# Optimization experiments

Hardware: AMD Instinct MI355X
Metric: run time of the kernel (lower is better)

The kernel has to match this reference:

```python
import jax, jax.numpy as jnp
import numpy as np
import math

N, L, D = 1024, 32, 768
N_OUT, IN_DIM, OUT_DIM = 16, 64, 64
EPS = 1e-8


def setup_inputs() -> dict:
    key = jax.random.key(0)
    ks = jax.random.split(key, 4)
    x = jax.random.normal(ks[0], (N, L, D), jnp.float32)
    mask = jnp.ones((N, L), jnp.float32)
    scaled = lambda k, shape, fan: jax.random.normal(k, shape, jnp.float32) * (1.0 / np.sqrt(fan).astype(np.float32))
    Wscore = scaled(ks[1], (L, D, 1), D)
    Bscore = jnp.zeros((L, 1, 1), jnp.float32)
    Wcap = scaled(ks[2], (L, D, IN_DIM), D)
    Bcap = jnp.zeros((L, 1, IN_DIM), jnp.float32)
    Wvote = scaled(ks[3], (L, N_OUT, IN_DIM, OUT_DIM), IN_DIM)
    Bvote = jnp.zeros((L, N_OUT, 1, OUT_DIM), jnp.float32)
    beta_use = jnp.zeros((L, 1, 1, 1), jnp.float32)
    beta_ign = jnp.zeros((1, N_OUT, 1, 1), jnp.float32)
    return dict(x=x, mask=mask, Wscore=Wscore, Bscore=Bscore, Wcap=Wcap,
                Bcap=Bcap, Wvote=Wvote, Bvote=Bvote, beta_use=beta_use,
                beta_ign=beta_ign, iters=3)


def reference(x, mask, Wscore, Bscore, Wcap, Bcap, Wvote, Bvote, beta_use, beta_ign, iters):
    n_out = Wvote.shape[1]
    half_pi = np.float32(0.5 * math.pi)
    x_t = jnp.transpose(x, (1, 0, 2))                      # [L, N, D]
    a_in = jnp.matmul(x_t, Wscore) + Bscore                # [L, N, 1]
    mu_in = jax.nn.gelu(jnp.matmul(x_t, Wcap) + Bcap, approximate=False)  # [L, N, in_dim]
    f_a_in = jax.nn.sigmoid(a_in) * jnp.transpose(mask)[..., None]        # [L, N, 1]
    f_a_in = f_a_in[:, None, :, :]                         # [L, 1, N, 1]
    # votes: [L, n_out, N, out_dim] (einsum avoids materializing repeated mu_in)
    V = jnp.einsum('lni,lkio->lkno', mu_in, Wvote) + Bvote

    R = jnp.full((1, n_out, 1, 1), 1.0 / n_out, dtype=x.dtype)
    a_out = mu_out = var_out = None
    for t in range(iters):
        if t > 0:
            log_p = (-jnp.sum((V - mu_out[None]) ** 2 / (2.0 * var_out[None] + EPS), axis=-1)
                     - 1.0 - half_pi
                     - 0.5 * jnp.sum(jnp.log(var_out[None] + EPS), axis=-1))   # [L, n_out, N]
            R = jax.nn.softmax(jax.nn.log_sigmoid(a_out)[None] + log_p[..., None], axis=1)
        D_use = f_a_in * R                                  # [L, n_out, N, 1]
        D_ign = f_a_in - D_use
        a_out = jnp.sum(beta_use * D_use, axis=0) - jnp.sum(beta_ign * D_ign, axis=0)  # [n_out, N, 1]
        denom = jnp.sum(D_use, axis=0) + EPS                # [n_out, N, 1]
        mu_out = jnp.sum(D_use * V, axis=0) / denom         # [n_out, N, out_dim]
        var_out = jnp.sum(D_use * (V - mu_out[None]) ** 2, axis=0) / denom

    a_fin = jnp.transpose(a_out[..., 0])                    # [N, n_out]
    mu_fin = jnp.transpose(mu_out, (1, 0, 2))               # [N, n_out, out_dim]
    return a_fin, mu_fin
```

## Files before the change

kernel.cpp:

```cpp
#include <hip/hip_runtime.h>
#include <hip/hip_bf16.h>

#define L_DIM 32
#define N_DIM 1024
#define D_DIM 768
#define K_DIM 16
#define I_DIM 64
#define O_DIM 64
#define EPSF 1e-8f
#define PX 72

typedef unsigned short u16;
typedef __attribute__((ext_vector_type(8))) short short8;
typedef __attribute__((ext_vector_type(4))) float f32x4;
#define MFMA __builtin_amdgcn_mfma_f32_16x16x32_bf16

__device__ __forceinline__ float bf2f(u16 v) {
    union { unsigned int u; float f; } x; x.u = ((unsigned int)v) << 16; return x.f;
}
__device__ __forceinline__ u16 f2bf(float f) {
    union { float f; unsigned int u; } x; x.f = f;
    unsigned int u = x.u;
    u += 0x7FFFu + ((u >> 16) & 1u);
    return (u16)(u >> 16);
}
__device__ __forceinline__ void split2(float v, u16& h, u16& l) {
    u16 hh = f2bf(v);
    h = hh;
    l = f2bf(v - bf2f(hh));
}
__device__ __forceinline__ void store_split4(u16* ph, u16* pl, float4 v) {
    unsigned u0 = __float_as_uint(v.x), u1 = __float_as_uint(v.y);
    unsigned u2 = __float_as_uint(v.z), u3 = __float_as_uint(v.w);
    uint2 H, L;
    H.x = (u0 >> 16) | (u1 & 0xFFFF0000u);
    H.y = (u2 >> 16) | (u3 & 0xFFFF0000u);
    float l0 = v.x - __uint_as_float(u0 & 0xFFFF0000u);
    float l1 = v.y - __uint_as_float(u1 & 0xFFFF0000u);
    float l2 = v.z - __uint_as_float(u2 & 0xFFFF0000u);
    float l3 = v.w - __uint_as_float(u3 & 0xFFFF0000u);
    L.x = (__float_as_uint(l0) >> 16) | (__float_as_uint(l1) & 0xFFFF0000u);
    L.y = (__float_as_uint(l2) >> 16) | (__float_as_uint(l3) & 0xFFFF0000u);
    *(uint2*)ph = H;
    *(uint2*)pl = L;
}

__global__ __launch_bounds__(256) void prep_wcap(
    const float* __restrict__ W, u16* __restrict__ H, u16* __restrict__ Lo)
{
    const int l = blockIdx.y, d0 = blockIdx.x * 64, t = threadIdx.x;
    __shared__ float tile[64][65];
    #pragma unroll
    for (int p = 0; p < 4; p++) {
        int dd = p * 16 + (t >> 4), i4 = (t & 15) * 4;
        float4 v = *(const float4*)&W[((size_t)l * D_DIM + d0 + dd) * I_DIM + i4];
        tile[dd][i4] = v.x; tile[dd][i4+1] = v.y; tile[dd][i4+2] = v.z; tile[dd][i4+3] = v.w;
    }
    __syncthreads();
    #pragma unroll
    for (int p = 0; p < 4; p++) {
        int i = p * 16 + (t >> 4), dd0 = (t & 15) * 4;
        u16 h[4], lo[4];
        #pragma unroll
        for (int j = 0; j < 4; j++) split2(tile[dd0 + j][i], h[j], lo[j]);
        size_t base = ((size_t)l * I_DIM + i) * D_DIM + d0 + dd0;
        uint2 ph; ph.x = h[0] | ((unsigned)h[1] << 16); ph.y = h[2] | ((unsigned)h[3] << 16);
        uint2 pl; pl.x = lo[0] | ((unsigned)lo[1] << 16); pl.y = lo[2] | ((unsigned)lo[3] << 16);
        *(uint2*)&H[base] = ph;
        *(uint2*)&Lo[base] = pl;
    }
}

__global__ __launch_bounds__(256) void prep_wvote(
    const float* __restrict__ W, u16* __restrict__ H, u16* __restrict__ Lo)
{
    const int l = blockIdx.y, k = blockIdx.x, t = threadIdx.x;
    __shared__ float tile[64][65];
    #pragma unroll
    for (int p = 0; p < 4; p++) {
        int i = p * 16 + (t >> 4), o4 = (t & 15) * 4;
        float4 v = *(const float4*)&W[(((size_t)l * K_DIM + k) * I_DIM + i) * O_DIM + o4];
        tile[i][o4] = v.x; tile[i][o4+1] = v.y; tile[i][o4+2] = v.z; tile[i][o4+3] = v.w;
    }
    __syncthreads();
    #pragma unroll
    for (int p = 0; p < 4; p++) {
        int o = p * 16 + (t >> 4), i0 = (t & 15) * 4;
        u16 h[4], lo[4];
        #pragma unroll
        for (int j = 0; j < 4; j++) split2(tile[i0 + j][o], h[j], lo[j]);
        size_t base = (((size_t)l * K_DIM + k) * O_DIM + o) * I_DIM + i0;
        uint2 ph; ph.x = h[0] | ((unsigned)h[1] << 16); ph.y = h[2] | ((unsigned)h[3] << 16);
        uint2 pl; pl.x = lo[0] | ((unsigned)lo[1] << 16); pl.y = lo[2] | ((unsigned)lo[3] << 16);
        *(uint2*)&H[base] = ph;
        *(uint2*)&Lo[base] = pl;
    }
}

__global__ __launch_bounds__(256) void kernelA(
    const float* __restrict__ x, const float* __restrict__ mask,
    const float* __restrict__ Wscore, const float* __restrict__ Bscore,
    const u16* __restrict__ WcH, const u16* __restrict__ WcL,
    const float* __restrict__ Bcap,
    float* __restrict__ mu_out, float* __restrict__ fa_out,
    int nbase, int nchunk)
{
    const int l   = blockIdx.y;
    const int n0l = blockIdx.x * 32;
    const int t    = threadIdx.x;
    const int w    = t >> 6;
    const int lane = t & 63;
    const int quad = lane >> 4;
    const int ln16 = lane & 15;

    __shared__ u16 xh[2][32][PX], xl[2][32][PX];
    __shared__ float wsc_s[D_DIM];
    __shared__ float bcap_s[64];

    for (int i = t; i < D_DIM; i += 256) wsc_s[i] = Wscore[l * D_DIM + i];
    if (t < 64) bcap_s[t] = Bcap[l * I_DIM + t];

    const int sg = t >> 4;
    const int sd = (t & 15) * 4;

    const size_t xoff0 = ((size_t)(nbase + n0l + sg) * L_DIM + l) * D_DIM + sd;
    const size_t xoff1 = ((size_t)(nbase + n0l + 16 + sg) * L_DIM + l) * D_DIM + sd;

    float4 xr0[12], xr1[12];
    #pragma unroll
    for (int ch = 0; ch < 12; ch++) {
        xr0[ch] = *(const float4*)&x[xoff0 + ch * 64];
        xr1[ch] = *(const float4*)&x[xoff1 + ch * 64];
    }

    __syncthreads();

    f32x4 acc[2] = {{0.f,0.f,0.f,0.f},{0.f,0.f,0.f,0.f}};
    float fa0 = 0.f, fa1 = 0.f;

    #pragma unroll
    for (int ch = 0; ch < 12; ch++) {
        const int buf = ch & 1;
        const int k0 = ch * 64;

        {
            const float* wp = &wsc_s[k0 + sd];
            fa0 += xr0[ch].x * wp[0] + xr0[ch].y * wp[1] + xr0[ch].z * wp[2] + xr0[ch].w * wp[3];
            fa1 += xr1[ch].x * wp[0] + xr1[ch].y * wp[1] + xr1[ch].z * wp[2] + xr1[ch].w * wp[3];
        }
        store_split4(&xh[buf][sg][sd],      &xl[buf][sg][sd],      xr0[ch]);
        store_split4(&xh[buf][16 + sg][sd], &xl[buf][16 + sg][sd], xr1[ch]);
        __syncthreads();

        #pragma unroll
        for (int ks = 0; ks < 2; ks++) {
            const int kk = ks * 32;
            size_t wbase = ((size_t)l * I_DIM + (w * 16 + ln16)) * D_DIM + k0 + kk + quad * 8;
            short8 ah = *(const short8*)&WcH[wbase];
            short8 al = *(const short8*)&WcL[wbase];
            #pragma unroll
            for (int c = 0; c < 2; c++) {
                const int n = c * 16 + ln16;
                short8 bh = *(const short8*)&xh[buf][n][kk + quad * 8];
                short8 bl = *(const short8*)&xl[buf][n][kk + quad * 8];
                acc[c] = MFMA(ah, bh, acc[c], 0, 0, 0);
                acc[c] = MFMA(ah, bl, acc[c], 0, 0, 0);
                acc[c] = MFMA(al, bh, acc[c], 0, 0, 0);
            }
        }
    }

    fa0 += __shfl_xor(fa0, 1, 64); fa1 += __shfl_xor(fa1, 1, 64);
    fa0 += __shfl_xor(fa0, 2, 64); fa1 += __shfl_xor(fa1, 2, 64);
    fa0 += __shfl_xor(fa0, 4, 64); fa1 += __shfl_xor(fa1, 4, 64);
    fa0 += __shfl_xor(fa0, 8, 64); fa1 += __shfl_xor(fa1, 8, 64);
    if ((t & 15) == 0) {
        float bs = Bscore[l];
        {
            float a = fa0 + bs;
            float sig = 1.f / (1.f + expf(-a));
            float m = mask[(size_t)(nbase + n0l + sg) * L_DIM + l];
            fa_out[(size_t)l * nchunk + n0l + sg] = sig * m;
        }
        {
            float a = fa1 + bs;
            float sig = 1.f / (1.f + expf(-a));
            float m = mask[(size_t)(nbase + n0l + 16 + sg) * L_DIM + l];
            fa_out[(size_t)l * nchunk + n0l + 16 + sg] = sig * m;
        }
    }

    #pragma unroll
    for (int c = 0; c < 2; c++) {
        const int n = c * 16 + ln16;
        const int i0 = w * 16 + quad * 4;
        float4 o;
        float* op = (float*)&o;
        #pragma unroll
        for (int r = 0; r < 4; r++) {
            float v = acc[c][r] + bcap_s[i0 + r];
            op[r] = 0.5f * v * (1.f + erff(v * 0.70710678118f));
        }
        *(float4*)&mu_out[((size_t)l * nchunk + n0l + n) * I_DIM + i0] = o;
    }
}

__global__ __launch_bounds__(256) void kernelB(
    const float* __restrict__ mu_in,
    const u16* __restrict__ WvH, const u16* __restrict__ WvL,
    const float* __restrict__ Bvote,
    float* __restrict__ V, int nchunk)
{
    const int l   = blockIdx.z;
    const int k   = blockIdx.y;
    const int n0l = blockIdx.x * 64;
    const int t    = threadIdx.x;
    const int w    = t >> 6;
    const int lane = t & 63;
    const int quad = lane >> 4;
    const int ln16 = lane & 15;

    __shared__ u16 mh[64][PX], ml[64][PX];
    __shared__ float bvote_s[64];

    if (t < 64) bvote_s[t] = Bvote[((size_t)l * K_DIM + k) * O_DIM + t];

    #pragma unroll
    for (int p = 0; p < 4; p++) {
        int n = p * 16 + (t >> 4), i0 = (t & 15) * 4;
        float4 v = *(const float4*)&mu_in[((size_t)l * nchunk + n0l + n) * I_DIM + i0];
        store_split4(&mh[n][i0], &ml[n][i0], v);
    }
    __syncthreads();

    f32x4 acc[4] = {{0.f,0.f,0.f,0.f},{0.f,0.f,0.f,0.f},{0.f,0.f,0.f,0.f},{0.f,0.f,0.f,0.f}};

    #pragma unroll
    for (int ks = 0; ks < 2; ks++) {
        const int kk = ks * 32;
        size_t wbase = (((size_t)l * K_DIM + k) * O_DIM + (w * 16 + ln16)) * I_DIM + kk + quad * 8;
        short8 ah = *(const short8*)&WvH[wbase];
        short8 al = *(const short8*)&WvL[wbase];
        #pragma unroll
        for (int c = 0; c < 4; c++) {
            const int n = c * 16 + ln16;
            short8 bh = *(const short8*)&mh[n][kk + quad * 8];
            short8 bl = *(const short8*)&ml[n][kk + quad * 8];
            acc[c] = MFMA(ah, bh, acc[c], 0, 0, 0);
            acc[c] = MFMA(ah, bl, acc[c], 0, 0, 0);
            acc[c] = MFMA(al, bh, acc[c], 0, 0, 0);
        }
    }

    #pragma unroll
    for (int c = 0; c < 4; c++) {
        const int n = c * 16 + ln16;
        const int o0 = w * 16 + quad * 4;
        float4 o;
        o.x = acc[c][0] + bvote_s[o0];
        o.y = acc[c][1] + bvote_s[o0 + 1];
        o.z = acc[c][2] + bvote_s[o0 + 2];
        o.w = acc[c][3] + bvote_s[o0 + 3];
        *(float4*)&V[(((size_t)l * K_DIM + k) * nchunk + n0l + n) * O_DIM + o0] = o;
    }
}

__global__ __launch_bounds__(256) void kernelC(
    const float* __restrict__ V, const float* __restrict__ fa_in,
    const float* __restrict__ beta_use, const float* __restrict__ beta_ign,
    const int* __restrict__ iters_p,
    float* __restrict__ out, int nbase, int nchunk)
{
    const int nl = blockIdx.x;
    const int ng = nbase + nl;
    const int t  = threadIdx.x;
    const int k  = t >> 4;
    const int og = (t & 15) << 2;

    __shared__ float fa_s[32];
    __shared__ float bu_s[32];
    __shared__ float R_s[32][17];
    __shared__ float sc_s[32][17];

    float Vr[32][4];
    #pragma unroll
    for (int l = 0; l < 32; l++) {
        float4 v = *(const float4*)&V[(((size_t)l * K_DIM + k) * nchunk + nl) * O_DIM + og];
        Vr[l][0] = v.x; Vr[l][1] = v.y; Vr[l][2] = v.z; Vr[l][3] = v.w;
    }

    int iters = iters_p[0];
    if (iters < 0 || iters > 16) iters = 3;

    if (t < 32) {
        fa_s[t] = fa_in[(size_t)t * nchunk + nl];
        bu_s[t] = beta_use[t];
    }
    for (int idx = t; idx < 512; idx += 256)
        R_s[idx >> 4][idx & 15] = 1.f / 16.f;
    const float bi_k = beta_ign[k];
    __syncthreads();

    float mu_r[4] = {0.f, 0.f, 0.f, 0.f};
    float var_r[4] = {0.f, 0.f, 0.f, 0.f};
    float a_r = 0.f;

    for (int it = 0; it < iters; it++) {
        if (it > 0) {
            float inv2v[4], lvp = 0.f;
            #pragma unroll
            for (int j = 0; j < 4; j++) {
                inv2v[j] = 1.f / (2.f * var_r[j] + EPSF);
                lvp += logf(var_r[j] + EPSF);
            }
            lvp += __shfl_xor(lvp, 1, 64);
            lvp += __shfl_xor(lvp, 2, 64);
            lvp += __shfl_xor(lvp, 4, 64);
            lvp += __shfl_xor(lvp, 8, 64);
            float ls = fminf(a_r, 0.f) - log1pf(expf(-fabsf(a_r)));
            const float cst = ls - 1.f - 1.57079632679f - 0.5f * lvp;
            #pragma unroll
            for (int l = 0; l < 32; l++) {
                float s = 0.f;
                #pragma unroll
                for (int j = 0; j < 4; j++) {
                    float d = Vr[l][j] - mu_r[j];
                    s += d * d * inv2v[j];
                }
                s = -s;
                s += __shfl_xor(s, 1, 64);
                s += __shfl_xor(s, 2, 64);
                s += __shfl_xor(s, 4, 64);
                s += __shfl_xor(s, 8, 64);
                if ((t & 15) == 0) sc_s[l][k] = s + cst;
            }
            __syncthreads();
            {
                const int lr = t >> 3;
                const int c2 = (t & 7) * 2;
                float s0 = sc_s[lr][c2], s1 = sc_s[lr][c2 + 1];
                float m = fmaxf(s0, s1);
                m = fmaxf(m, __shfl_xor(m, 1, 64));
                m = fmaxf(m, __shfl_xor(m, 2, 64));
                m = fmaxf(m, __shfl_xor(m, 4, 64));
                float e0 = expf(s0 - m), e1 = expf(s1 - m);
                float sum = e0 + e1;
                sum += __shfl_xor(sum, 1, 64);
                sum += __shfl_xor(sum, 2, 64);
                sum += __shfl_xor(sum, 4, 64);
                float inv = 1.f / sum;
                R_s[lr][c2]     = e0 * inv;
                R_s[lr][c2 + 1] = e1 * inv;
            }
            __syncthreads();
        }
        float denom = EPSF, a_acc = 0.f;
        float mu_a[4] = {0.f, 0.f, 0.f, 0.f};
        float v2_a[4] = {0.f, 0.f, 0.f, 0.f};
        #pragma unroll
        for (int l = 0; l < 32; l++) {
            float Du = fa_s[l] * R_s[l][k];
            denom += Du;
            a_acc += bu_s[l] * Du - bi_k * (fa_s[l] - Du);
            #pragma unroll
            for (int j = 0; j < 4; j++) {
                float dv = Du * Vr[l][j];
                mu_a[j] += dv;
                v2_a[j] += dv * Vr[l][j];
            }
        }
        float invd = 1.f / denom;
        #pragma unroll
        for (int j = 0; j < 4; j++) {
            mu_r[j] = mu_a[j] * invd;
            var_r[j] = fmaxf(v2_a[j] * invd - mu_r[j] * mu_r[j], 0.f);
        }
        a_r = a_acc;
    }

    if ((t & 15) == 0) out[(size_t)ng * K_DIM + k] = a_r;
    float4 o4;
    o4.x = mu_r[0]; o4.y = mu_r[1]; o4.z = mu_r[2]; o4.w = mu_r[3];
    *(float4*)&out[(size_t)N_DIM * K_DIM + ((size_t)ng * K_DIM + k) * O_DIM + og] = o4;
}

extern "C" void kernel_launch(void* const* d_in, const int* in_sizes, int n_in,
                              void* d_out, int out_size, void* d_ws, size_t ws_size,
                              hipStream_t stream) {
    (void)out_size;
    static const int EXP[11] = {25165824, 32768, 24576, 32, 1572864, 64,
                                2097152, 65536, 32, 16, 1};
    int mapi[11];
    bool used[64] = {false};
    for (int s = 0; s < 11; s++) {
        mapi[s] = (s < n_in) ? s : 0;
        for (int j = 0; j < n_in && j < 64; j++) {
            if (!used[j] && in_sizes[j] == EXP[s]) { mapi[s] = j; used[j] = true; break; }
        }
    }
    const float* x        = (const float*)d_in[mapi[0]];
    const float* mask     = (const float*)d_in[mapi[1]];
    const float* Wscore   = (const float*)d_in[mapi[2]];
    const float* Bscore   = (const float*)d_in[mapi[3]];
    const float* Wcap     = (const float*)d_in[mapi[4]];
    const float* Bcap     = (const float*)d_in[mapi[5]];
    const float* Wvote    = (const float*)d_in[mapi[6]];
    const float* Bvote    = (const float*)d_in[mapi[7]];
    const float* beta_use = (const float*)d_in[mapi[8]];
    const float* beta_ign = (const float*)d_in[mapi[9]];
    const int*   iters    = (const int*)d_in[mapi[10]];
    float* out = (float*)d_out;

    const size_t WCAP = (size_t)L_DIM * I_DIM * D_DIM;
    const size_t WVOT = (size_t)L_DIM * K_DIM * O_DIM * I_DIM;
    const size_t WBYTES = 2 * WCAP * 2 + 2 * WVOT * 2;

    int C = 64;
    {
        const int cands[5] = {1024, 512, 256, 128, 64};
        for (int i = 0; i < 5; i++) {
            size_t need = WBYTES + (size_t)cands[i] * (128 + 8192 + 131072);
            if (need <= ws_size) { C = cands[i]; break; }
        }
    }

    char* ws = (char*)d_ws;
    u16* WcH = (u16*)ws;
    u16* WcL = (u16*)(ws + WCAP * 2);
    u16* WvH = (u16*)(ws + WCAP * 4);
    u16* WvL = (u16*)(ws + WCAP * 4 + WVOT * 2);
    char* dyn = ws + WBYTES;
    float* fa = (float*)dyn;
    float* mu = (float*)(dyn + (size_t)128 * C);
    float* V  = (float*)(dyn + (size_t)128 * C + (size_t)8192 * C);

    prep_wcap<<<dim3(12, 32), 256, 0, stream>>>(Wcap, WcH, WcL);
    prep_wvote<<<dim3(16, 32), 256, 0, stream>>>(Wvote, WvH, WvL);

    for (int nbase = 0; nbase < N_DIM; nbase += C) {
        kernelA<<<dim3(C / 32, 32), 256, 0, stream>>>(
            x, mask, Wscore, Bscore, WcH, WcL, Bcap, mu, fa, nbase, C);
        kernelB<<<dim3(C / 64, 16, 32), 256, 0, stream>>>(
            mu, WvH, WvL, Bvote, V, C);
        kernelC<<<dim3(C), 256, 0, stream>>>(
            V, fa, beta_use, beta_ign, iters, out, nbase, C);
    }
}
```

Baseline: 308.6 us.

## Load x directly into MFMA registers in kernelA, dropping LDS staging

Result: slower. 354.1 us (+14.7%).

```diff
diff --git a/kernel.cpp b/kernel.cpp
--- a/kernel.cpp
+++ b/kernel.cpp
@@ -44,6 +44,18 @@
     *(uint2*)ph = H;
     *(uint2*)pl = L;
 }
+__device__ __forceinline__ void split8r(float4 v0, float4 v1, short8& h, short8& l) {
+    union { short8 s; u16 u[8]; } H, L;
+    float vv[8] = {v0.x, v0.y, v0.z, v0.w, v1.x, v1.y, v1.z, v1.w};
+    #pragma unroll
+    for (int j = 0; j < 8; j++) {
+        unsigned u = __float_as_uint(vv[j]);
+        H.u[j] = (u16)(u >> 16);
+        float lo = vv[j] - __uint_as_float(u & 0xFFFF0000u);
+        L.u[j] = (u16)(__float_as_uint(lo) >> 16);
+    }
+    h = H.s; l = L.s;
+}
 
 __global__ __launch_bounds__(256) void prep_wcap(
     const float* __restrict__ W, u16* __restrict__ H, u16* __restrict__ Lo)
@@ -106,103 +118,64 @@
     int nbase, int nchunk)
 {
     const int l   = blockIdx.y;
-    const int n0l = blockIdx.x * 32;
+    const int n0l = blockIdx.x * 16;
     const int t    = threadIdx.x;
     const int w    = t >> 6;
     const int lane = t & 63;
     const int quad = lane >> 4;
     const int ln16 = lane & 15;
 
-    __shared__ u16 xh[2][32][PX], xl[2][32][PX];
     __shared__ float wsc_s[D_DIM];
     __shared__ float bcap_s[64];
 
     for (int i = t; i < D_DIM; i += 256) wsc_s[i] = Wscore[l * D_DIM + i];
     if (t < 64) bcap_s[t] = Bcap[l * I_DIM + t];
-
-    const int sg = t >> 4;
-    const int sd = (t & 15) * 4;
-
-    const size_t xoff0 = ((size_t)(nbase + n0l + sg) * L_DIM + l) * D_DIM + sd;
-    const size_t xoff1 = ((size_t)(nbase + n0l + 16 + sg) * L_DIM + l) * D_DIM + sd;
-
-    float4 xr0[12], xr1[12];
-    #pragma unroll
-    for (int ch = 0; ch < 12; ch++) {
-        xr0[ch] = *(const float4*)&x[xoff0 + ch * 64];
-        xr1[ch] = *(const float4*)&x[xoff1 + ch * 64];
-    }
-
     __syncthreads();
 
-    f32x4 acc[2] = {{0.f,0.f,0.f,0.f},{0.f,0.f,0.f,0.f}};
-    float fa0 = 0.f, fa1 = 0.f;
-
-    #pragma unroll
-    for (int ch = 0; ch < 12; ch++) {
-        const int buf = ch & 1;
-        const int k0 = ch * 64;
-
-        {
-            const float* wp = &wsc_s[k0 + sd];
-            fa0 += xr0[ch].x * wp[0] + xr0[ch].y * wp[1] + xr0[ch].z * wp[2] + xr0[ch].w * wp[3];
-            fa1 += xr1[ch].x * wp[0] + xr1[ch].y * wp[1] + xr1[ch].z * wp[2] + xr1[ch].w * wp[3];
-        }
-        store_split4(&xh[buf][sg][sd],      &xl[buf][sg][sd],      xr0[ch]);
-        store_split4(&xh[buf][16 + sg][sd], &xl[buf][16 + sg][sd], xr1[ch]);
-        __syncthreads();
-
-        #pragma unroll
-        for (int ks = 0; ks < 2; ks++) {
-            const int kk = ks * 32;
-            size_t wbase = ((size_t)l * I_DIM + (w * 16 + ln16)) * D_DIM + k0 + kk + quad * 8;
-            short8 ah = *(const short8*)&WcH[wbase];
-            short8 al = *(const short8*)&WcL[wbase];
-            #pragma unroll
-            for (int c = 0; c < 2; c++) {
-                const int n = c * 16 + ln16;
-                short8 bh = *(const short8*)&xh[buf][n][kk + quad * 8];
-                short8 bl = *(const short8*)&xl[buf][n][kk + quad * 8];
-                acc[c] = MFMA(ah, bh, acc[c], 0, 0, 0);
-                acc[c] = MFMA(ah, bl, acc[c], 0, 0, 0);
-                acc[c] = MFMA(al, bh, acc[c], 0, 0, 0);
-            }
-        }
-    }
-
-    fa0 += __shfl_xor(fa0, 1, 64); fa1 += __shfl_xor(fa1, 1, 64);
-    fa0 += __shfl_xor(fa0, 2, 64); fa1 += __shfl_xor(fa1, 2, 64);
-    fa0 += __shfl_xor(fa0, 4, 64); fa1 += __shfl_xor(fa1, 4, 64);
-    fa0 += __shfl_xor(fa0, 8, 64); fa1 += __shfl_xor(fa1, 8, 64);
-    if ((t & 15) == 0) {
-        float bs = Bscore[l];
-        {
-            float a = fa0 + bs;
-            float sig = 1.f / (1.f + expf(-a));
-            float m = mask[(size_t)(nbase + n0l + sg) * L_DIM + l];
-            fa_out[(size_t)l * nchunk + n0l + sg] = sig * m;
-        }
-        {
-            float a = fa1 + bs;
-            float sig = 1.f / (1.f + expf(-a));
-            float m = mask[(size_t)(nbase + n0l + 16 + sg) * L_DIM + l];
-            fa_out[(size_t)l * nchunk + n0l + 16 + sg] = sig * m;
-        }
-    }
-
-    #pragma unroll
-    for (int c = 0; c < 2; c++) {
-        const int n = c * 16 + ln16;
-        const int i0 = w * 16 + quad * 4;
-        float4 o;
-        float* op = (float*)&o;
-        #pragma unroll
-        for (int r = 0; r < 4; r++) {
-            float v = acc[c][r] + bcap_s[i0 + r];
-            op[r] = 0.5f * v * (1.f + erff(v * 0.70710678118f));
-        }
-        *(float4*)&mu_out[((size_t)l * nchunk + n0l + n) * I_DIM + i0] = o;
-    }
+    const float* xrow  = &x[((size_t)(nbase + n0l + ln16) * L_DIM + l) * D_DIM];
+    const u16*   whrow = &WcH[((size_t)l * I_DIM + (w * 16 + ln16)) * D_DIM];
+    const u16*   wlrow = &WcL[((size_t)l * I_DIM + (w * 16 + ln16)) * D_DIM];
+
+    f32x4 acc = {0.f, 0.f, 0.f, 0.f};
+    float fap = 0.f;
+
+    #pragma unroll
+    for (int ks = 0; ks < 24; ks++) {
+        const int d0 = ks * 32 + quad * 8;
+        float4 xv0 = *(const float4*)&xrow[d0];
+        float4 xv1 = *(const float4*)&xrow[d0 + 4];
+        short8 ah = *(const short8*)&whrow[d0];
+        short8 al = *(const short8*)&wlrow[d0];
+
+        const float* wp = &wsc_s[d0];
+        fap += xv0.x * wp[0] + xv0.y * wp[1] + xv0.z * wp[2] + xv0.w * wp[3]
+             + xv1.x * wp[4] + xv1.y * wp[5] + xv1.z * wp[6] + xv1.w * wp[7];
+
+        short8 bh, bl;
+        split8r(xv0, xv1, bh, bl);
+        acc = MFMA(ah, bh, acc, 0, 0, 0);
+        acc = MFMA(ah, bl, acc, 0, 0, 0);
+        acc = MFMA(al, bh, acc, 0, 0, 0);
+    }
+
+    fap += __shfl_xor(fap, 16, 64);
+    fap += __shfl_xor(fap, 32, 64);
+    if (w == 0 && lane < 16) {
+        float a = fap + Bscore[l];
+        float sig = 1.f / (1.f + expf(-a));
+        float m = mask[(size_t)(nbase + n0l + lane) * L_DIM + l];
+        fa_out[(size_t)l * nchunk + n0l + lane] = sig * m;
+    }
+
+    const int i0 = w * 16 + quad * 4;
+    float4 o;
+    float* op = (float*)&o;
+    #pragma unroll
+    for (int r = 0; r < 4; r++) {
+        float v = acc[r] + bcap_s[i0 + r];
+        op[r] = 0.5f * v * (1.f + erff(v * 0.70710678118f));
+    }
+    *(float4*)&mu_out[((size_t)l * nchunk + n0l + ln16) * I_DIM + i0] = o;
 }
 
 __global__ __launch_bounds__(256) void kernelB(
@@ -438,7 +411,7 @@
     prep_wvote<<<dim3(16, 32), 256, 0, stream>>>(Wvote, WvH, WvL);
 
     for (int nbase = 0; nbase < N_DIM; nbase += C) {
-        kernelA<<<dim3(C / 32, 32), 256, 0, stream>>>(
+        kernelA<<<dim3(C / 16, 32), 256, 0, stream>>>(
             x, mask, Wscore, Bscore, WcH, WcL, Bcap, mu, fa, nbase, C);
         kernelB<<<dim3(C / 64, 16, 32), 256, 0, stream>>>(
             mu, WvH, WvL, Bvote, V, C);
```
